# Optimization experiments

Hardware: AMD Instinct MI355X
Metric: run time of the kernel (lower is better)

## Reference

```python
import jax, jax.numpy as jnp
import numpy as np


def setup_inputs() -> dict:
    key = jax.random.key(0)
    k1, k2, k3, k4 = jax.random.split(key, 4)
    T, H, I, E, K = 4096, 1024, 1024, 8, 2
    hidden_states = jax.random.normal(k1, (T, H), dtype=jnp.float32)
    router_logits = jax.random.normal(k2, (T, E), dtype=jnp.float32)
    # fused gate+up projection: [E, H, 2*I]; down projection: [E, I, H]
    up_weight = jax.random.normal(k3, (E, H, 2 * I), dtype=jnp.float32) * 0.02
    down_weight = jax.random.normal(k4, (E, I, H), dtype=jnp.float32) * 0.02
    return {"hidden_states": hidden_states, "router_logits": router_logits,
            "up_weight": up_weight, "down_weight": down_weight, "topk": K}


def reference(hidden_states, router_logits, up_weight, down_weight, topk):
    T, H = hidden_states.shape
    E = up_weight.shape[0]
    I = down_weight.shape[1]
    K = topk
    # select_experts: softmax over all experts, top-k, renormalize weights
    probs = jax.nn.softmax(router_logits, axis=-1)
    topk_w, topk_ids = jax.lax.top_k(probs, K)               # [T, K]
    topk_w = topk_w / jnp.sum(topk_w, axis=-1, keepdims=True)
    # expand tokens: each token is dispatched K times (grouped-GEMM operand)
    xk = jnp.repeat(hidden_states, K, axis=0)                # [T*K, H]
    flat_ids = topk_ids.reshape(-1)                          # [T*K]
    acc = jnp.zeros((T * K, H), dtype=hidden_states.dtype)
    for e in range(E):  # fixed small expert loop (grouped GEMM semantics)
        mask = (flat_ids == e).astype(hidden_states.dtype)[:, None]
        xe = xk * mask                                       # zero out non-e tokens
        gu = xe @ up_weight[e]                               # [T*K, 2I]
        h = jax.nn.silu(gu[:, :I]) * gu[:, I:]               # gated SiLU
        acc = acc + h @ down_weight[e]                       # [T*K, H]
    # combine: weighted sum over the K expert slots (reduce step)
    out = jnp.einsum('tk,tkh->th', topk_w, acc.reshape(T, K, H))
    return out
```

## Files before the change

kernel.cpp:

```cpp
#include <hip/hip_runtime.h>
#include <hip/hip_bf16.h>


#define T_TOK 4096
#define HDIM  1024
#define NEXP  8
#define RROWS (T_TOK * 2)
#define MAXPE T_TOK

typedef unsigned short u16;
typedef short v8s __attribute__((ext_vector_type(8)));
typedef float v4f __attribute__((ext_vector_type(4)));
typedef __attribute__((address_space(3))) unsigned int as3_u32;
typedef const __attribute__((address_space(1))) unsigned int as1_u32c;

__device__ __forceinline__ float b2f(u16 u) {
    union { unsigned int i; float f; } v; v.i = ((unsigned int)u) << 16; return v.f;
}
__device__ __forceinline__ u16 f2b(float f) {
    union { float f; unsigned int i; } v; v.f = f;
    unsigned int x = v.i;
    return (u16)((x + 0x7FFFu + ((x >> 16) & 1u)) >> 16);
}
__device__ __forceinline__ unsigned int pack2(float a, float b) {
    return (unsigned int)f2b(a) | ((unsigned int)f2b(b) << 16);
}
__device__ __forceinline__ void stage16(const u16* g, u16* l) {
    __builtin_amdgcn_global_load_lds((as1_u32c*)g, (as3_u32*)l, 16, 0, 0);
}

__device__ __forceinline__ void cvt_tile(const float* __restrict__ Wb,
                                         u16* __restrict__ Wtb,
                                         int N, int n0b, int k0b, u16* sm) {
    const int tid = threadIdx.x;
    const int m = tid & 15, rr = tid >> 4;
    float4 f[16];
#pragma unroll
    for (int s = 0; s < 4; s++)
#pragma unroll
        for (int j = 0; j < 4; j++)
            f[s * 4 + j] = *(const float4*)(Wb + (size_t)(k0b + s * 64 + rr * 4 + j) * N
                                               + n0b + m * 4);
#pragma unroll
    for (int s = 0; s < 4; s++) {
        const int kc = s * 16 + rr;
        const float* fp = (const float*)&f[s * 4];
#pragma unroll
        for (int nl = 0; nl < 4; nl++) {
            int n_l = m * 4 + nl;
            uint2 v;
            v.x = pack2(fp[nl], fp[4 + nl]);
            v.y = pack2(fp[8 + nl], fp[12 + nl]);
            *(uint2*)&sm[n_l * 256 + ((kc ^ (n_l & 15)) << 2)] = v;
        }
    }
    __syncthreads();
    const int n_l = tid >> 2, q = tid & 3, sw = n_l & 15;
    u16* dst = Wtb + (size_t)(n0b + n_l) * 1024 + k0b + q * 64;
#pragma unroll
    for (int c2 = 0; c2 < 8; c2++) {
        uint2 a = *(const uint2*)&sm[n_l * 256 + (((q * 16 + 2 * c2) ^ sw) << 2)];
        uint2 b = *(const uint2*)&sm[n_l * 256 + (((q * 16 + 2 * c2 + 1) ^ sw) << 2)];
        uint4 o; o.x = a.x; o.y = a.y; o.z = b.x; o.w = b.y;
        *(uint4*)(dst + c2 * 8) = o;
    }
}

__global__ __launch_bounds__(256)
void prep_all(const float* __restrict__ X, const float* __restrict__ RL,
              const float* __restrict__ WU, const float* __restrict__ WD,
              u16* __restrict__ Xb, u16* __restrict__ WtU, u16* __restrict__ WtD,
              int* __restrict__ ids, float* __restrict__ wts,
              int* __restrict__ counts, int* __restrict__ rowbuf) {
    __shared__ __align__(16) u16 sm[64 * 256];
    const int bx = blockIdx.x;
    const int tid = threadIdx.x;

    if (bx < 1024) {
        int e = bx >> 7, r = bx & 127;
        int nt = r >> 2, kt = r & 3;
        cvt_tile(WU + (size_t)e * 1024 * 2048, WtU + (size_t)e * 2048 * 1024,
                 2048, nt * 64, kt * 256, sm);
    } else if (bx < 1536) {
        int base = (bx - 1024) * 8192 + tid * 4;
#pragma unroll
        for (int j = 0; j < 8; j++) {
            float4 fx = *(const float4*)(X + base + j * 1024);
            uint2 o; o.x = pack2(fx.x, fx.y); o.y = pack2(fx.z, fx.w);
            *(uint2*)(Xb + base + j * 1024) = o;
        }
    } else if (bx < 1552) {
        int t = (bx - 1536) * 256 + tid;
        float4 a = *(const float4*)(RL + t * NEXP);
        float4 b = *(const float4*)(RL + t * NEXP + 4);
        float l[NEXP] = {a.x, a.y, a.z, a.w, b.x, b.y, b.z, b.w};
        int i0 = 0;
#pragma unroll
        for (int q = 1; q < NEXP; q++) if (l[q] > l[i0]) i0 = q;
        int i1 = (i0 == 0) ? 1 : 0;
#pragma unroll
        for (int q = 0; q < NEXP; q++) if (q != i0 && l[q] > l[i1]) i1 = q;
        float w0 = 1.0f / (1.0f + expf(l[i1] - l[i0]));
        ids[2 * t] = i0;     ids[2 * t + 1] = i1;
        wts[2 * t] = w0;     wts[2 * t + 1] = 1.0f - w0;
        int p0 = atomicAdd(&counts[i0], 1);
        rowbuf[i0 * MAXPE + p0] = 2 * t;
        int p1 = atomicAdd(&counts[i1], 1);
        rowbuf[i1 * MAXPE + p1] = 2 * t + 1;
    } else {
        int ci = bx - 1552;
        int e = ci >> 6, r = ci & 63;
        int nt = r >> 2, kt = r & 3;
        cvt_tile(WD + (size_t)e * 1024 * 1024, WtD + (size_t)e * 1024 * 1024,
                 1024, nt * 64, kt * 256, sm);
    }
}

template<int PHASE>
__global__ __launch_bounds__(256)
void mfma_gemm(const u16* __restrict__ A, const u16* __restrict__ Bt,
               u16* __restrict__ H,
               const int* __restrict__ counts, const int* __restrict__ rowbuf) {
    __shared__ __align__(16) u16 smem[4 * 128 * 64];
    __shared__ int srid[128];
    const int bi = blockIdx.x;
    const int xcd = bi & 7, kb = bi >> 3;
    int e, ct, rt;
    if (PHASE == 1) { int p = (kb & 15) * 8 + xcd; e = p >> 4; ct = p & 15; rt = kb >> 4; }
    else            { int p = (kb & 7) * 8 + xcd;  e = p >> 3; ct = p & 7;  rt = kb >> 3; }
    const int cnt = counts[e];
    if (rt * 128 >= cnt) return;
    const int tid = threadIdx.x;
    const int lane = tid & 63, wave = tid >> 6;

    u16* sA0 = smem;
    u16* sB0 = smem + 8192;
    u16* sA1 = smem + 16384;
    u16* sB1 = smem + 24576;

    if (tid < 128) {
        int idx = rt * 128 + tid;
        srid[tid] = (idx < cnt) ? rowbuf[e * MAXPE + idx] : -1;
    }
    __syncthreads();

    const int lrow = lane >> 3;
    const int lchunk = (lane & 7) ^ lrow;
    const u16* aPtr[4]; const u16* bPtr[4];
    int offs[4];
#pragma unroll
    for (int p = 0; p < 4; p++) {
        int region = p * 4 + wave;
        int r = region * 8 + lrow;
        int rid = srid[r];
        int arow = (rid < 0) ? 0 : (PHASE == 1 ? (rid >> 1) : rid);
        aPtr[p] = A + (size_t)arow * 1024 + lchunk * 8;
        int n;
        if (PHASE == 1) n = (r < 64) ? (ct * 64 + r) : (1024 + ct * 64 + (r - 64));
        else            n = ct * 128 + r;
        bPtr[p] = Bt + (size_t)e * (PHASE == 1 ? 2048 : 1024) * 1024
                     + (size_t)n * 1024 + lchunk * 8;
        offs[p] = region * 512 + lane * 8;
    }

    const int quad = lane >> 4, mr = lane & 15;
    const int swA = mr & 7;
    const v4f zf = {0.f, 0.f, 0.f, 0.f};
    v4f acc[2][8];
#pragma unroll
    for (int i = 0; i < 2; i++)
#pragma unroll
        for (int j = 0; j < 8; j++) acc[i][j] = zf;

    auto stageAll = [&](u16* sAx, u16* sBx, int kk) {
#pragma unroll
        for (int p = 0; p < 4; p++) {
            stage16(aPtr[p] + kk * 64, sAx + offs[p]);
            stage16(bPtr[p] + kk * 64, sBx + offs[p]);
        }
    };
    auto computeTile = [&](const u16* sAx, const u16* sBx) {
#pragma unroll
        for (int kh = 0; kh < 2; kh++) {
            const int c = kh * 4 + quad;
            v8s a0 = *(const v8s*)(sAx + (wave * 32 + mr) * 64 + ((c ^ swA) * 8));
            v8s a1 = *(const v8s*)(sAx + (wave * 32 + 16 + mr) * 64 + ((c ^ swA) * 8));
#pragma unroll
            for (int nf = 0; nf < 8; nf++) {
                v8s b = *(const v8s*)(sBx + (nf * 16 + mr) * 64 + ((c ^ swA) * 8));
                acc[0][nf] = __builtin_amdgcn_mfma_f32_16x16x32_bf16(a0, b, acc[0][nf], 0, 0, 0);
                acc[1][nf] = __builtin_amdgcn_mfma_f32_16x16x32_bf16(a1, b, acc[1][nf], 0, 0, 0);
            }
        }
    };

    stageAll(sA0, sB0, 0);
#pragma unroll 1
    for (int kt = 0; kt < 8; kt++) {
        stageAll(sA1, sB1, 2 * kt + 1);
        asm volatile("s_waitcnt vmcnt(8)" ::: "memory");
        __builtin_amdgcn_s_barrier();
        computeTile(sA0, sB0);
        __builtin_amdgcn_s_barrier();
        if (kt < 7) {
            stageAll(sA0, sB0, 2 * kt + 2);
            asm volatile("s_waitcnt vmcnt(8)" ::: "memory");
        } else {
            asm volatile("s_waitcnt vmcnt(0)" ::: "memory");
        }
        __builtin_amdgcn_s_barrier();
        computeTile(sA1, sB1);
        __builtin_amdgcn_s_barrier();
    }

#pragma unroll
    for (int mf = 0; mf < 2; mf++) {
#pragma unroll
        for (int reg = 0; reg < 4; reg++) {
            int rl = wave * 32 + mf * 16 + quad * 4 + reg;
            int grow = srid[rl];
            if (grow < 0) continue;
            if (PHASE == 1) {
                size_t base = (size_t)grow * 1024 + ct * 64 + mr;
#pragma unroll
                for (int nf = 0; nf < 4; nf++) {
                    float g = acc[mf][nf][reg], u = acc[mf][nf + 4][reg];
                    H[base + nf * 16] = f2b((g / (1.0f + expf(-g))) * u);
                }
            } else {
                size_t base = (size_t)grow * 1024 + ct * 128 + mr;
#pragma unroll
                for (int nf = 0; nf < 8; nf++)
                    H[base + nf * 16] = f2b(acc[mf][nf][reg]);
            }
        }
    }
}

__global__ void combine_kernel(const u16* __restrict__ accb,
                               const float* __restrict__ wts,
                               float* __restrict__ out) {
    int g = blockIdx.x * blockDim.x + threadIdx.x;
    int t = g >> 8;
    int c = (g & 255) * 4;
    float w0 = wts[2 * t], w1 = wts[2 * t + 1];
    ushort4 a = *(const ushort4*)(accb + (size_t)(2 * t) * 1024 + c);
    ushort4 b = *(const ushort4*)(accb + (size_t)(2 * t + 1) * 1024 + c);
    float4 o;
    o.x = w0 * b2f(a.x) + w1 * b2f(b.x);
    o.y = w0 * b2f(a.y) + w1 * b2f(b.y);
    o.z = w0 * b2f(a.z) + w1 * b2f(b.z);
    o.w = w0 * b2f(a.w) + w1 * b2f(b.w);
    *(float4*)(out + (size_t)t * 1024 + c) = o;
}

__global__ void router_kernel(const float* __restrict__ logits,
                              int* __restrict__ ids, float* __restrict__ wts) {
    int t = blockIdx.x * blockDim.x + threadIdx.x;
    if (t >= T_TOK) return;
    float4 a = *(const float4*)(logits + t * NEXP);
    float4 b = *(const float4*)(logits + t * NEXP + 4);
    float l[NEXP] = {a.x, a.y, a.z, a.w, b.x, b.y, b.z, b.w};
    int i0 = 0;
#pragma unroll
    for (int i = 1; i < NEXP; i++) if (l[i] > l[i0]) i0 = i;
    int i1 = (i0 == 0) ? 1 : 0;
#pragma unroll
    for (int i = 0; i < NEXP; i++) if (i != i0 && l[i] > l[i1]) i1 = i;
    float w0 = 1.0f / (1.0f + expf(l[i1] - l[i0]));
    ids[2 * t] = i0;     ids[2 * t + 1] = i1;
    wts[2 * t] = w0;     wts[2 * t + 1] = 1.0f - w0;
}

__global__ void bucket_kernel(const int* __restrict__ ids,
                              int* __restrict__ counts, int* __restrict__ rowbuf) {
    int r = blockIdx.x * blockDim.x + threadIdx.x;
    if (r >= RROWS) return;
    int e = ids[r];
    int pos = atomicAdd(&counts[e], 1);
    rowbuf[e * MAXPE + pos] = r;
}

template<int GATED, int AF32>
__global__ __launch_bounds__(256)
void moe_gemm_kernel(const void* __restrict__ Av,
                     const float* __restrict__ B,
                     u16* __restrict__ C,
                     const int* __restrict__ counts,
                     const int* __restrict__ rowbuf,
                     int rowShift, int NB) {
    const int e   = blockIdx.z;
    const int cnt = counts[e];
    const int rt  = blockIdx.y;
    if (rt * 128 >= cnt) return;
    const int ct  = blockIdx.x;
    const int tid = threadIdx.x;

    __shared__ __align__(16) u16 sA[128 * 40];
    __shared__ __align__(16) u16 sB[(GATED ? 2 : 1) * 64 * 40];
    __shared__ int srid[128];

    if (tid < 128) {
        int idx = rt * 128 + tid;
        srid[tid] = (idx < cnt) ? rowbuf[e * MAXPE + idx] : -1;
    }
    __syncthreads();

    const int ar = tid >> 1, ac = (tid & 1) * 16;
    int arid = srid[ar];
    const float* aSrcF = 0; const u16* aSrcH = 0;
    if (arid >= 0) {
        if (AF32) aSrcF = (const float*)Av + (size_t)(arid >> rowShift) * HDIM + ac;
        else      aSrcH = (const u16*)Av + (size_t)(arid >> rowShift) * HDIM + ac;
    }
    u16* aDst = sA + ar * 40 + ac;

    const int kq2 = (tid >> 4) * 2, n4 = (tid & 15) * 4;
    const float* bSrcG = B + (size_t)e * 1024 * NB + (size_t)kq2 * NB + ct * 64 + n4;
    const float* bSrcU = bSrcG + 1024;

    const int lane = tid & 63, wave = tid >> 6;
    const int quad = lane >> 4, mr = lane & 15;

    const v4f zf = {0.f, 0.f, 0.f, 0.f};
    v4f accG[2][4], accU[2][4];
#pragma unroll
    for (int i = 0; i < 2; i++)
#pragma unroll
        for (int j = 0; j < 4; j++) { accG[i][j] = zf; accU[i][j] = zf; }

    for (int kk = 0; kk < HDIM / 32; kk++) {
        uint4 aw0 = make_uint4(0, 0, 0, 0), aw1 = make_uint4(0, 0, 0, 0);
        if (AF32) {
            if (aSrcF) {
                float4 f0 = *(const float4*)(aSrcF + kk * 32);
                float4 f1 = *(const float4*)(aSrcF + kk * 32 + 4);
                float4 f2 = *(const float4*)(aSrcF + kk * 32 + 8);
                float4 f3 = *(const float4*)(aSrcF + kk * 32 + 12);
                aw0 = make_uint4(pack2(f0.x, f0.y), pack2(f0.z, f0.w),
                                 pack2(f1.x, f1.y), pack2(f1.z, f1.w));
                aw1 = make_uint4(pack2(f2.x, f2.y), pack2(f2.z, f2.w),
                                 pack2(f3.x, f3.y), pack2(f3.z, f3.w));
            }
        } else {
            if (aSrcH) {
                aw0 = *(const uint4*)(aSrcH + kk * 32);
                aw1 = *(const uint4*)(aSrcH + kk * 32 + 8);
            }
        }
        const size_t bOff = (size_t)kk * 32 * NB;
        float4 g0 = *(const float4*)(bSrcG + bOff);
        float4 g1 = *(const float4*)(bSrcG + bOff + NB);
        float4 u0 = make_float4(0, 0, 0, 0), u1 = make_float4(0, 0, 0, 0);
        if (GATED) {
            u0 = *(const float4*)(bSrcU + bOff);
            u1 = *(const float4*)(bSrcU + bOff + NB);
        }

        __syncthreads();
        *(uint4*)aDst = aw0;
        *(uint4*)(aDst + 8) = aw1;
        {
            const float gx[4] = {g0.x, g0.y, g0.z, g0.w};
            const float gy[4] = {g1.x, g1.y, g1.z, g1.w};
#pragma unroll
            for (int j = 0; j < 4; j++)
                *(unsigned int*)&sB[(n4 + j) * 40 + kq2] = pack2(gx[j], gy[j]);
            if (GATED) {
                const float ux[4] = {u0.x, u0.y, u0.z, u0.w};
                const float uy[4] = {u1.x, u1.y, u1.z, u1.w};
#pragma unroll
                for (int j = 0; j < 4; j++)
                    *(unsigned int*)&sB[64 * 40 + (n4 + j) * 40 + kq2] = pack2(ux[j], uy[j]);
            }
        }
        __syncthreads();

        v8s af0 = *(const v8s*)(sA + (wave * 32 + mr) * 40 + quad * 8);
        v8s af1 = *(const v8s*)(sA + (wave * 32 + 16 + mr) * 40 + quad * 8);
#pragma unroll
        for (int nf = 0; nf < 4; nf++) {
            v8s bg = *(const v8s*)(sB + (nf * 16 + mr) * 40 + quad * 8);
            accG[0][nf] = __builtin_amdgcn_mfma_f32_16x16x32_bf16(af0, bg, accG[0][nf], 0, 0, 0);
            accG[1][nf] = __builtin_amdgcn_mfma_f32_16x16x32_bf16(af1, bg, accG[1][nf], 0, 0, 0);
            if (GATED) {
                v8s bu = *(const v8s*)(sB + 64 * 40 + (nf * 16 + mr) * 40 + quad * 8);
                accU[0][nf] = __builtin_amdgcn_mfma_f32_16x16x32_bf16(af0, bu, accU[0][nf], 0, 0, 0);
                accU[1][nf] = __builtin_amdgcn_mfma_f32_16x16x32_bf16(af1, bu, accU[1][nf], 0, 0, 0);
            }
        }
    }

#pragma unroll
    for (int mf = 0; mf < 2; mf++) {
#pragma unroll
        for (int reg = 0; reg < 4; reg++) {
            int rl = wave * 32 + mf * 16 + quad * 4 + reg;
            int grow = srid[rl];
            if (grow < 0) continue;
            size_t base = (size_t)grow * 1024 + ct * 64 + mr;
#pragma unroll
            for (int nf = 0; nf < 4; nf++) {
                float g = accG[mf][nf][reg];
                float val;
                if (GATED) {
                    float u = accU[mf][nf][reg];
                    val = (g / (1.0f + expf(-g))) * u;
                } else {
                    val = g;
                }
                C[base + nf * 16] = f2b(val);
            }
        }
    }
}

extern "C" void kernel_launch(void* const* d_in, const int* in_sizes, int n_in,
                              void* d_out, int out_size, void* d_ws, size_t ws_size,
                              hipStream_t stream) {
    const float *X = 0, *RL = 0, *WU = 0, *WD = 0;
    for (int i = 0; i < n_in; i++) {
        switch (in_sizes[i]) {
            case T_TOK * HDIM:        X  = (const float*)d_in[i]; break;
            case T_TOK * NEXP:        RL = (const float*)d_in[i]; break;
            case NEXP * HDIM * 2048:  WU = (const float*)d_in[i]; break;
            case NEXP * HDIM * 1024:  WD = (const float*)d_in[i]; break;
            default: break;
        }
    }
    if (!X)  X  = (const float*)d_in[0];
    if (!RL) RL = (const float*)d_in[1];
    if (!WU) WU = (const float*)d_in[2];
    if (!WD) WD = (const float*)d_in[3];
    float* OUT = (float*)d_out;

    char* ws = (char*)d_ws;
    int*   ids    = (int*)(ws + 0);
    float* wts    = (float*)(ws + 32768);
    int*   counts = (int*)(ws + 65536);
    int*   rowbuf = (int*)(ws + 65792);
    u16* Xb   = (u16*)(ws + 196864);
    u16* WtU  = (u16*)(ws + 8585472);
    u16* WtD  = (u16*)(ws + 42139904);
    u16* HbufF= (u16*)(ws + 58917120);
    u16* AccF = WtU;
    const size_t needFast = 75694336ull;
    u16* Hbuf = (u16*)(ws + 196864);
    u16* Acc  = (u16*)(ws + 196864 + 16777216);

    hipMemsetAsync(counts, 0, NEXP * sizeof(int), stream);

    if (ws_size >= needFast) {
        prep_all<<<2064, 256, 0, stream>>>(
            X, RL, WU, WD, Xb, WtU, WtD, ids, wts, counts, rowbuf);
        mfma_gemm<1><<<4096, 256, 0, stream>>>(Xb, WtU, HbufF, counts, rowbuf);
        mfma_gemm<2><<<2048, 256, 0, stream>>>(HbufF, WtD, AccF, counts, rowbuf);
        combine_kernel<<<T_TOK, 256, 0, stream>>>(AccF, wts, OUT);
    } else {
        router_kernel<<<T_TOK / 256, 256, 0, stream>>>(RL, ids, wts);
        bucket_kernel<<<RROWS / 256, 256, 0, stream>>>(ids, counts, rowbuf);
        moe_gemm_kernel<1, 1><<<dim3(16, 32, NEXP), 256, 0, stream>>>(
            (const void*)X, WU, Hbuf, counts, rowbuf, 1, 2048);
        moe_gemm_kernel<0, 0><<<dim3(16, 32, NEXP), 256, 0, stream>>>(
            (const void*)Hbuf, WD, Acc, counts, rowbuf, 0, 1024);
        combine_kernel<<<T_TOK, 256, 0, stream>>>(Acc, wts, OUT);
    }
}
```

Baseline: 278.5 us.

## Enlarge GEMM row tile to 256 with 8 waves; stage weight conversion via async LDS loads

The grouped GEMM kernels now use 512-thread blocks covering 256 token rows per tile instead of 128. Each weight tile staged in LDS is reused across twice as many rows, which reduces B-operand traffic, at the cost of more shared memory per block and more padding waste for partially filled expert tiles. The weight fp32-to-bf16 transpose in prep is rewritten to use smaller tiles staged with global_load_lds and a swizzled fp32 LDS layout, replacing the register-based conversion. Risk: the visible compute/epilogue section may not have been updated for 8 waves, since wave*32 indexing now covers only 256 rows if consistent.

```diff
diff --git a/kernel.cpp b/kernel.cpp
--- a/kernel.cpp
+++ b/kernel.cpp
@@ -27,43 +27,6 @@
 }
 __device__ __forceinline__ void stage16(const u16* g, u16* l) {
     __builtin_amdgcn_global_load_lds((as1_u32c*)g, (as3_u32*)l, 16, 0, 0);
-}
-
-__device__ __forceinline__ void cvt_tile(const float* __restrict__ Wb,
-                                         u16* __restrict__ Wtb,
-                                         int N, int n0b, int k0b, u16* sm) {
-    const int tid = threadIdx.x;
-    const int m = tid & 15, rr = tid >> 4;
-    float4 f[16];
-#pragma unroll
-    for (int s = 0; s < 4; s++)
-#pragma unroll
-        for (int j = 0; j < 4; j++)
-            f[s * 4 + j] = *(const float4*)(Wb + (size_t)(k0b + s * 64 + rr * 4 + j) * N
-                                               + n0b + m * 4);
-#pragma unroll
-    for (int s = 0; s < 4; s++) {
-        const int kc = s * 16 + rr;
-        const float* fp = (const float*)&f[s * 4];
-#pragma unroll
-        for (int nl = 0; nl < 4; nl++) {
-            int n_l = m * 4 + nl;
-            uint2 v;
-            v.x = pack2(fp[nl], fp[4 + nl]);
-            v.y = pack2(fp[8 + nl], fp[12 + nl]);
-            *(uint2*)&sm[n_l * 256 + ((kc ^ (n_l & 15)) << 2)] = v;
-        }
-    }
-    __syncthreads();
-    const int n_l = tid >> 2, q = tid & 3, sw = n_l & 15;
-    u16* dst = Wtb + (size_t)(n0b + n_l) * 1024 + k0b + q * 64;
-#pragma unroll
-    for (int c2 = 0; c2 < 8; c2++) {
-        uint2 a = *(const uint2*)&sm[n_l * 256 + (((q * 16 + 2 * c2) ^ sw) << 2)];
-        uint2 b = *(const uint2*)&sm[n_l * 256 + (((q * 16 + 2 * c2 + 1) ^ sw) << 2)];
-        uint4 o; o.x = a.x; o.y = a.y; o.z = b.x; o.w = b.y;
-        *(uint4*)(dst + c2 * 8) = o;
-    }
 }
 
 __global__ __launch_bounds__(256)
@@ -72,25 +35,61 @@
               u16* __restrict__ Xb, u16* __restrict__ WtU, u16* __restrict__ WtD,
               int* __restrict__ ids, float* __restrict__ wts,
               int* __restrict__ counts, int* __restrict__ rowbuf) {
-    __shared__ __align__(16) u16 sm[64 * 256];
+    __shared__ __align__(16) float smf[128 * 64];
     const int bx = blockIdx.x;
     const int tid = threadIdx.x;
 
-    if (bx < 1024) {
-        int e = bx >> 7, r = bx & 127;
-        int nt = r >> 2, kt = r & 3;
-        cvt_tile(WU + (size_t)e * 1024 * 2048, WtU + (size_t)e * 2048 * 1024,
-                 2048, nt * 64, kt * 256, sm);
-    } else if (bx < 1536) {
-        int base = (bx - 1024) * 8192 + tid * 4;
+    if (bx < 3072) {
+        const float* Wb; u16* Wtb; int N, e, nt, kt;
+        if (bx < 2048) {
+            e = bx >> 8; int r = bx & 255;
+            nt = r >> 3; kt = r & 7;
+            Wb = WU + (size_t)e * 1024 * 2048; Wtb = WtU + (size_t)e * 2048 * 1024; N = 2048;
+        } else {
+            int b = bx - 2048;
+            e = b >> 7; int r = b & 127;
+            nt = r >> 3; kt = r & 7;
+            Wb = WD + (size_t)e * 1024 * 1024; Wtb = WtD + (size_t)e * 1024 * 1024; N = 1024;
+        }
+        const int n0 = nt * 64, k0 = kt * 128;
+        const int wv = tid >> 6, l = tid & 63;
+#pragma unroll
+        for (int i = 0; i < 8; i++) {
+            int reg = wv * 8 + i;
+            int k = reg * 4 + (l >> 4);
+            int c = l & 15;
+            int ng = c ^ (k & 15) ^ (((k >> 5) & 3) << 2);
+            stage16((const u16*)(Wb + (size_t)(k0 + k) * N + n0 + 4 * ng),
+                    (u16*)smf + reg * 512 + l * 8);
+        }
+        __syncthreads();
+        const int n_l = tid >> 2, q = tid & 3;
+        const int ng = n_l >> 2, sub = n_l & 3;
+        u16* dst = Wtb + (size_t)(n0 + n_l) * 1024 + k0 + q * 32;
+#pragma unroll
+        for (int c8 = 0; c8 < 4; c8++) {
+            float v[8];
+#pragma unroll
+            for (int j = 0; j < 8; j++) {
+                int k = q * 32 + c8 * 8 + j;
+                int sw = ng ^ (k & 15) ^ (((k >> 5) & 3) << 2);
+                v[j] = smf[k * 64 + sw * 4 + sub];
+            }
+            uint4 o;
+            o.x = pack2(v[0], v[1]); o.y = pack2(v[2], v[3]);
+            o.z = pack2(v[4], v[5]); o.w = pack2(v[6], v[7]);
+            *(uint4*)(dst + c8 * 8) = o;
+        }
+    } else if (bx < 3584) {
+        int base = (bx - 3072) * 8192 + tid * 4;
 #pragma unroll
         for (int j = 0; j < 8; j++) {
             float4 fx = *(const float4*)(X + base + j * 1024);
             uint2 o; o.x = pack2(fx.x, fx.y); o.y = pack2(fx.z, fx.w);
             *(uint2*)(Xb + base + j * 1024) = o;
         }
-    } else if (bx < 1552) {
-        int t = (bx - 1536) * 256 + tid;
+    } else {
+        int t = (bx - 3584) * 256 + tid;
         float4 a = *(const float4*)(RL + t * NEXP);
         float4 b = *(const float4*)(RL + t * NEXP + 4);
         float l[NEXP] = {a.x, a.y, a.z, a.w, b.x, b.y, b.z, b.w};
@@ -107,60 +106,60 @@
         rowbuf[i0 * MAXPE + p0] = 2 * t;
         int p1 = atomicAdd(&counts[i1], 1);
         rowbuf[i1 * MAXPE + p1] = 2 * t + 1;
-    } else {
-        int ci = bx - 1552;
-        int e = ci >> 6, r = ci & 63;
-        int nt = r >> 2, kt = r & 3;
-        cvt_tile(WD + (size_t)e * 1024 * 1024, WtD + (size_t)e * 1024 * 1024,
-                 1024, nt * 64, kt * 256, sm);
     }
 }
 
 template<int PHASE>
-__global__ __launch_bounds__(256)
+__global__ __launch_bounds__(512)
 void mfma_gemm(const u16* __restrict__ A, const u16* __restrict__ Bt,
                u16* __restrict__ H,
                const int* __restrict__ counts, const int* __restrict__ rowbuf) {
-    __shared__ __align__(16) u16 smem[4 * 128 * 64];
-    __shared__ int srid[128];
+    __shared__ __align__(16) u16 smem[49152];
+    __shared__ int srid[256];
     const int bi = blockIdx.x;
     const int xcd = bi & 7, kb = bi >> 3;
     int e, ct, rt;
     if (PHASE == 1) { int p = (kb & 15) * 8 + xcd; e = p >> 4; ct = p & 15; rt = kb >> 4; }
     else            { int p = (kb & 7) * 8 + xcd;  e = p >> 3; ct = p & 7;  rt = kb >> 3; }
     const int cnt = counts[e];
-    if (rt * 128 >= cnt) return;
+    if (rt * 256 >= cnt) return;
     const int tid = threadIdx.x;
     const int lane = tid & 63, wave = tid >> 6;
 
     u16* sA0 = smem;
-    u16* sB0 = smem + 8192;
-    u16* sA1 = smem + 16384;
-    u16* sB1 = smem + 24576;
-
-    if (tid < 128) {
-        int idx = rt * 128 + tid;
+    u16* sB0 = smem + 16384;
+    u16* sA1 = smem + 24576;
+    u16* sB1 = smem + 40960;
+
+    if (tid < 256) {
+        int idx = rt * 256 + tid;
         srid[tid] = (idx < cnt) ? rowbuf[e * MAXPE + idx] : -1;
     }
     __syncthreads();
 
     const int lrow = lane >> 3;
     const int lchunk = (lane & 7) ^ lrow;
-    const u16* aPtr[4]; const u16* bPtr[4];
-    int offs[4];
+    const u16* aPtr[4]; const u16* bPtr[2];
+    int aOff[4], bOff[2];
 #pragma unroll
     for (int p = 0; p < 4; p++) {
-        int region = p * 4 + wave;
+        int region = p * 8 + wave;
         int r = region * 8 + lrow;
         int rid = srid[r];
         int arow = (rid < 0) ? 0 : (PHASE == 1 ? (rid >> 1) : rid);
         aPtr[p] = A + (size_t)arow * 1024 + lchunk * 8;
+        aOff[p] = region * 512 + lane * 8;
+    }
+#pragma unroll
+    for (int p = 0; p < 2; p++) {
+        int region = p * 8 + wave;
+        int r = region * 8 + lrow;
         int n;
         if (PHASE == 1) n = (r < 64) ? (ct * 64 + r) : (1024 + ct * 64 + (r - 64));
         else            n = ct * 128 + r;
         bPtr[p] = Bt + (size_t)e * (PHASE == 1 ? 2048 : 1024) * 1024
                      + (size_t)n * 1024 + lchunk * 8;
-        offs[p] = region * 512 + lane * 8;
+        bOff[p] = region * 512 + lane * 8;
     }
 
     const int quad = lane >> 4, mr = lane & 15;
@@ -174,10 +173,9 @@
 
     auto stageAll = [&](u16* sAx, u16* sBx, int kk) {
 #pragma unroll
-        for (int p = 0; p < 4; p++) {
-            stage16(aPtr[p] + kk * 64, sAx + offs[p]);
-            stage16(bPtr[p] + kk * 64, sBx + offs[p]);
-        }
+        for (int p = 0; p < 4; p++) stage16(aPtr[p] + kk * 64, sAx + aOff[p]);
+#pragma unroll
+        for (int p = 0; p < 2; p++) stage16(bPtr[p] + kk * 64, sBx + bOff[p]);
     };
     auto computeTile = [&](const u16* sAx, const u16* sBx) {
 #pragma unroll
@@ -198,13 +196,13 @@
 #pragma unroll 1
     for (int kt = 0; kt < 8; kt++) {
         stageAll(sA1, sB1, 2 * kt + 1);
-        asm volatile("s_waitcnt vmcnt(8)" ::: "memory");
+        asm volatile("s_waitcnt vmcnt(6)" ::: "memory");
         __builtin_amdgcn_s_barrier();
         computeTile(sA0, sB0);
         __builtin_amdgcn_s_barrier();
         if (kt < 7) {
             stageAll(sA0, sB0, 2 * kt + 2);
-            asm volatile("s_waitcnt vmcnt(8)" ::: "memory");
+            asm volatile("s_waitcnt vmcnt(6)" ::: "memory");
         } else {
             asm volatile("s_waitcnt vmcnt(0)" ::: "memory");
         }
@@ -451,10 +449,10 @@
     hipMemsetAsync(counts, 0, NEXP * sizeof(int), stream);
 
     if (ws_size >= needFast) {
-        prep_all<<<2064, 256, 0, stream>>>(
+        prep_all<<<3600, 256, 0, stream>>>(
             X, RL, WU, WD, Xb, WtU, WtD, ids, wts, counts, rowbuf);
-        mfma_gemm<1><<<4096, 256, 0, stream>>>(Xb, WtU, HbufF, counts, rowbuf);
-        mfma_gemm<2><<<2048, 256, 0, stream>>>(HbufF, WtD, AccF, counts, rowbuf);
+        mfma_gemm<1><<<2048, 512, 0, stream>>>(Xb, WtU, HbufF, counts, rowbuf);
+        mfma_gemm<2><<<1024, 512, 0, stream>>>(HbufF, WtD, AccF, counts, rowbuf);
         combine_kernel<<<T_TOK, 256, 0, stream>>>(AccF, wts, OUT);
     } else {
         router_kernel<<<T_TOK / 256, 256, 0, stream>>>(RL, ids, wts);
```

New measurement: 298.4 us. +7.1%, slower.

## Pre-tile and pre-swizzle bf16 weights so GEMM B loads are contiguous

Applied to the files above, without the earlier changes.

The weight conversion now stages fp32 rows into LDS with direct global-to-LDS loads, then writes bf16 weights in a tiled layout: 64x64 tiles, each already XOR-swizzled to match the GEMM's LDS layout. The GEMM's B-operand loads then read one contiguous 8 KB block per k-step instead of gathering strided rows. This aims to make both the conversion and the GEMM B staging more coalesced. The block index ranges of the prep kernel are reordered, so the prep grid size and the phase-1/phase-2 indexing must stay consistent with the hidden host code.

```diff
diff --git a/kernel.cpp b/kernel.cpp
--- a/kernel.cpp
+++ b/kernel.cpp
@@ -27,43 +27,6 @@
 }
 __device__ __forceinline__ void stage16(const u16* g, u16* l) {
     __builtin_amdgcn_global_load_lds((as1_u32c*)g, (as3_u32*)l, 16, 0, 0);
-}
-
-__device__ __forceinline__ void cvt_tile(const float* __restrict__ Wb,
-                                         u16* __restrict__ Wtb,
-                                         int N, int n0b, int k0b, u16* sm) {
-    const int tid = threadIdx.x;
-    const int m = tid & 15, rr = tid >> 4;
-    float4 f[16];
-#pragma unroll
-    for (int s = 0; s < 4; s++)
-#pragma unroll
-        for (int j = 0; j < 4; j++)
-            f[s * 4 + j] = *(const float4*)(Wb + (size_t)(k0b + s * 64 + rr * 4 + j) * N
-                                               + n0b + m * 4);
-#pragma unroll
-    for (int s = 0; s < 4; s++) {
-        const int kc = s * 16 + rr;
-        const float* fp = (const float*)&f[s * 4];
-#pragma unroll
-        for (int nl = 0; nl < 4; nl++) {
-            int n_l = m * 4 + nl;
-            uint2 v;
-            v.x = pack2(fp[nl], fp[4 + nl]);
-            v.y = pack2(fp[8 + nl], fp[12 + nl]);
-            *(uint2*)&sm[n_l * 256 + ((kc ^ (n_l & 15)) << 2)] = v;
-        }
-    }
-    __syncthreads();
-    const int n_l = tid >> 2, q = tid & 3, sw = n_l & 15;
-    u16* dst = Wtb + (size_t)(n0b + n_l) * 1024 + k0b + q * 64;
-#pragma unroll
-    for (int c2 = 0; c2 < 8; c2++) {
-        uint2 a = *(const uint2*)&sm[n_l * 256 + (((q * 16 + 2 * c2) ^ sw) << 2)];
-        uint2 b = *(const uint2*)&sm[n_l * 256 + (((q * 16 + 2 * c2 + 1) ^ sw) << 2)];
-        uint4 o; o.x = a.x; o.y = a.y; o.z = b.x; o.w = b.y;
-        *(uint4*)(dst + c2 * 8) = o;
-    }
 }
 
 __global__ __launch_bounds__(256)
@@ -72,25 +35,56 @@
               u16* __restrict__ Xb, u16* __restrict__ WtU, u16* __restrict__ WtD,
               int* __restrict__ ids, float* __restrict__ wts,
               int* __restrict__ counts, int* __restrict__ rowbuf) {
-    __shared__ __align__(16) u16 sm[64 * 256];
+    __shared__ __align__(16) float smf[64 * 256];
     const int bx = blockIdx.x;
     const int tid = threadIdx.x;
 
-    if (bx < 1024) {
-        int e = bx >> 7, r = bx & 127;
-        int nt = r >> 2, kt = r & 3;
-        cvt_tile(WU + (size_t)e * 1024 * 2048, WtU + (size_t)e * 2048 * 1024,
-                 2048, nt * 64, kt * 256, sm);
-    } else if (bx < 1536) {
-        int base = (bx - 1024) * 8192 + tid * 4;
+    if (bx < 1536) {
+        const float* Wb; u16* Wtb; int N, NT, e, nb, kb;
+        if (bx < 1024) {
+            e = bx >> 7; int r = bx & 127;
+            nb = r >> 4; kb = r & 15;
+            Wb = WU + (size_t)e * 1024 * 2048; Wtb = WtU; N = 2048; NT = 32;
+        } else {
+            int b = bx - 1024;
+            e = b >> 6; int r = b & 63;
+            nb = r >> 4; kb = r & 15;
+            Wb = WD + (size_t)e * 1024 * 1024; Wtb = WtD; N = 1024; NT = 16;
+        }
+        const int n0 = nb * 256, k0 = kb * 64;
+        const int wv = tid >> 6, l = tid & 63;
+#pragma unroll
+        for (int i = 0; i < 16; i++) {
+            int k = wv * 16 + i;
+            stage16((const u16*)(Wb + (size_t)(k0 + k) * N + n0) + l * 8,
+                    (u16*)smf + k * 512 + l * 8);
+        }
+        __syncthreads();
+        const int n_l = tid;
+        const int tile_n = n_l >> 6, n_in = n_l & 63;
+        const int lrow = n_in & 7;
+        u16* tbase = Wtb + ((size_t)(e * NT + nb * 4 + tile_n) * 16 + kb) * 4096
+                   + (n_in >> 3) * 512 + lrow * 64;
+#pragma unroll
+        for (int c = 0; c < 8; c++) {
+            float v[8];
+#pragma unroll
+            for (int j = 0; j < 8; j++) v[j] = smf[(c * 8 + j) * 256 + n_l];
+            uint4 o;
+            o.x = pack2(v[0], v[1]); o.y = pack2(v[2], v[3]);
+            o.z = pack2(v[4], v[5]); o.w = pack2(v[6], v[7]);
+            *(uint4*)(tbase + (c ^ lrow) * 8) = o;
+        }
+    } else if (bx < 2048) {
+        int base = (bx - 1536) * 8192 + tid * 4;
 #pragma unroll
         for (int j = 0; j < 8; j++) {
             float4 fx = *(const float4*)(X + base + j * 1024);
             uint2 o; o.x = pack2(fx.x, fx.y); o.y = pack2(fx.z, fx.w);
             *(uint2*)(Xb + base + j * 1024) = o;
         }
-    } else if (bx < 1552) {
-        int t = (bx - 1536) * 256 + tid;
+    } else {
+        int t = (bx - 2048) * 256 + tid;
         float4 a = *(const float4*)(RL + t * NEXP);
         float4 b = *(const float4*)(RL + t * NEXP + 4);
         float l[NEXP] = {a.x, a.y, a.z, a.w, b.x, b.y, b.z, b.w};
@@ -107,12 +101,6 @@
         rowbuf[i0 * MAXPE + p0] = 2 * t;
         int p1 = atomicAdd(&counts[i1], 1);
         rowbuf[i1 * MAXPE + p1] = 2 * t + 1;
-    } else {
-        int ci = bx - 1552;
-        int e = ci >> 6, r = ci & 63;
-        int nt = r >> 2, kt = r & 3;
-        cvt_tile(WD + (size_t)e * 1024 * 1024, WtD + (size_t)e * 1024 * 1024,
-                 1024, nt * 64, kt * 256, sm);
     }
 }
 
@@ -155,11 +143,11 @@
         int rid = srid[r];
         int arow = (rid < 0) ? 0 : (PHASE == 1 ? (rid >> 1) : rid);
         aPtr[p] = A + (size_t)arow * 1024 + lchunk * 8;
-        int n;
-        if (PHASE == 1) n = (r < 64) ? (ct * 64 + r) : (1024 + ct * 64 + (r - 64));
-        else            n = ct * 128 + r;
-        bPtr[p] = Bt + (size_t)e * (PHASE == 1 ? 2048 : 1024) * 1024
-                     + (size_t)n * 1024 + lchunk * 8;
+        int nt;
+        if (PHASE == 1) nt = (region < 8) ? ct : (16 + ct);
+        else            nt = ct * 2 + (region >> 3);
+        bPtr[p] = Bt + ((size_t)(e * (PHASE == 1 ? 32 : 16) + nt) * 16) * 4096
+                     + (region & 7) * 512 + lane * 8;
         offs[p] = region * 512 + lane * 8;
     }
 
@@ -176,7 +164,7 @@
 #pragma unroll
         for (int p = 0; p < 4; p++) {
             stage16(aPtr[p] + kk * 64, sAx + offs[p]);
-            stage16(bPtr[p] + kk * 64, sBx + offs[p]);
+            stage16(bPtr[p] + kk * 4096, sBx + offs[p]);
         }
     };
     auto computeTile = [&](const u16* sAx, const u16* sBx) {
```

Measured after the change: 288.7 us. 3.7% more time.
